# Kernel optimization log

Hardware: AMD Instinct MI355X
Metric: run time of the kernel (lower is better)

## Reference

```python
import jax, jax.numpy as jnp
import numpy as np

BN_EPS = 1e-5
INTERP_EPS = 1e-8


def _bn_relu(x, g, b, m, v):
    # eval-mode BatchNorm1d over channel dim (last axis here) + ReLU
    return jax.nn.relu((x - m) * (g / jnp.sqrt(v + BN_EPS)) + b)


def setup_inputs() -> dict:
    key = jax.random.key(0)
    ks = jax.random.split(key, 12)
    B, N, S, C1, C2 = 4, 16384, 1024, 128, 256
    Cin = C1 + C2  # 384
    H1, H2 = 256, 128
    inp = {
        "xyz1": jax.random.normal(ks[0], (B, N, 3), jnp.float32),
        "xyz2": jax.random.normal(ks[1], (B, S, 3), jnp.float32),
        "points1": jax.random.normal(ks[2], (B, N, C1), jnp.float32),
        "points2": jax.random.normal(ks[3], (B, S, C2), jnp.float32),
        # Conv1d(k=1, bias=False) weights: (out_ch, in_ch)
        "w1": jax.random.normal(ks[4], (H1, Cin), jnp.float32) * (1.0 / np.sqrt(Cin)),
        "g1": jax.random.uniform(ks[5], (H1,), jnp.float32, 0.5, 1.5),
        "b1": jax.random.normal(ks[6], (H1,), jnp.float32) * 0.1,
        "m1": jax.random.normal(ks[7], (H1,), jnp.float32) * 0.1,
        "v1": jax.random.uniform(ks[8], (H1,), jnp.float32, 0.5, 1.5),
        "w2": jax.random.normal(ks[9], (H2, H1), jnp.float32) * (1.0 / np.sqrt(H1)),
        "g2": jax.random.uniform(ks[10], (H2,), jnp.float32, 0.5, 1.5),
        "b2": jax.random.normal(ks[11], (H2,), jnp.float32) * 0.1,
        "m2": jnp.zeros((H2,), jnp.float32),
        "v2": jnp.ones((H2,), jnp.float32),
    }
    return inp


def reference(xyz1, xyz2, points1, points2, w1, g1, b1, m1, v1, w2, g2, b2, m2, v2):
    B, N, _ = xyz1.shape
    S = xyz2.shape[1]
    # squared pairwise distances (B, N, S) via ||a||^2 + ||b||^2 - 2 a.b
    sq = (
        jnp.sum(xyz1 * xyz1, -1)[:, :, None]
        + jnp.sum(xyz2 * xyz2, -1)[:, None, :]
        - 2.0 * jnp.einsum("bnd,bsd->bns", xyz1, xyz2)
    )
    neg_d, idx = jax.lax.top_k(-sq, 3)  # 3 nearest neighbors
    dists = -neg_d  # (B, N, 3) squared distances, ascending
    recip = 1.0 / (dists + INTERP_EPS)
    weight = recip / jnp.sum(recip, -1, keepdims=True)  # (B, N, 3)
    # gather neighbor features: (B, N, 3, C2)
    gathered = points2[jnp.arange(B)[:, None, None], idx]
    interpolated = jnp.einsum("bnk,bnkc->bnc", weight, gathered)
    new_points = jnp.concatenate([points1, interpolated], axis=-1)  # (B, N, Cin)
    h = _bn_relu(jnp.einsum("bnc,dc->bnd", new_points, w1), g1, b1, m1, v1)
    out = _bn_relu(jnp.einsum("bnc,dc->bnd", h, w2), g2, b2, m2, v2)
    return out
```

## Files before the change

### kernel.cpp

```cpp
#include <hip/hip_runtime.h>
#include <math.h>

#define B_    4
#define N_    16384
#define S_    1024
#define C1_   128
#define C2_   256
#define CIN_  384
#define H1_   256
#define H2_   128
#define BN_EPS_     1e-5f
#define INTERP_EPS_ 1e-8f

typedef _Float16 f16;
typedef _Float16 f16x4 __attribute__((ext_vector_type(4)));
typedef _Float16 f16x8 __attribute__((ext_vector_type(8)));
typedef float    f32x4 __attribute__((ext_vector_type(4)));
typedef unsigned int u32;

#define GLD16(g, l) \
  __builtin_amdgcn_global_load_lds((const __attribute__((address_space(1))) void*)(g), \
                                   (__attribute__((address_space(3))) void*)(l), 16, 0, 0)

#define WS_IDXP 0
#define WS_W    262144
#define WS_XI   1048576
#define WS_H    34603008
#define WS_W1F  68157440
#define WS_W2F  68354048
#define WS_SC1  68419584
#define WS_SH1  68420608
#define WS_SC2  68421632
#define WS_SH2  68422144

__global__ __launch_bounds__(256) void prep_kernel(
    const float* __restrict__ w1, const float* __restrict__ w2,
    const float* __restrict__ g1, const float* __restrict__ b1,
    const float* __restrict__ m1, const float* __restrict__ v1,
    const float* __restrict__ g2, const float* __restrict__ b2,
    const float* __restrict__ m2, const float* __restrict__ v2,
    f16* __restrict__ w1f, f16* __restrict__ w2f,
    float* __restrict__ sc1, float* __restrict__ sh1,
    float* __restrict__ sc2, float* __restrict__ sh2)
{
    const int t = blockIdx.x * 256 + threadIdx.x;
    if (t < 98304) {
        w1f[t] = (f16)w1[t];
    } else if (t < 131072) {
        w2f[t - 98304] = (f16)w2[t - 98304];
    } else if (t < 131328) {
        const int c = t - 131072;
        const float s = g1[c] / sqrtf(v1[c] + BN_EPS_);
        sc1[c] = s; sh1[c] = b1[c] - m1[c] * s;
    } else if (t < 131456) {
        const int c = t - 131328;
        const float s = g2[c] / sqrtf(v2[c] + BN_EPS_);
        sc2[c] = s; sh2[c] = b2[c] - m2[c] * s;
    }
}

__device__ __forceinline__ u32 umin_(u32 a, u32 b) { return a < b ? a : b; }
__device__ __forceinline__ u32 umax_(u32 a, u32 b) { return a > b ? a : b; }

#define KINS(k) do { \
    u32 c1 = umax_(s0, (k)); s0 = umin_(s0, (k)); \
    u32 c2 = umax_(s1, c1);  s1 = umin_(s1, c1);  \
    u32 c3 = umax_(s2, c2);  s2 = umin_(s2, c2);  \
    u32 c4 = umax_(s3, c3);  s3 = umin_(s3, c3);  \
    s4 = umin_(s4, c4); } while (0)

#define CSWAP(a_, b_) do { \
    if (rd[b_] < rd[a_] || (rd[b_] == rd[a_] && ri[b_] < ri[a_])) { \
      double td = rd[a_]; rd[a_] = rd[b_]; rd[b_] = td; \
      int ti = ri[a_]; ri[a_] = ri[b_]; ri[b_] = ti; } } while (0)

__global__ __launch_bounds__(256) void topk_kernel(
    const float* __restrict__ xyz1, const float* __restrict__ xyz2,
    u32* __restrict__ idxp_out, float* __restrict__ w_out)
{
    __shared__ float4 q[S_ + 8];
    const int b     = blockIdx.x >> 9;
    const int pbase = (blockIdx.x & 511) << 5;
    const int t     = threadIdx.x;

    for (int i = t; i < S_; i += 256) {
        const float* s = &xyz2[((size_t)b * S_ + i) * 3];
        float4 v; v.x = s[0]; v.y = s[1]; v.z = s[2]; v.w = 0.0f;
        q[i + (i >> 7)] = v;
    }
    __syncthreads();

    const int p     = pbase + (t >> 3);
    const int chunk = t & 7;
    const int qb    = chunk * 129;
    const int ebase = chunk << 7;
    const float* pp = &xyz1[((size_t)b * N_ + p) * 3];
    const float px = pp[0], py = pp[1], pz = pp[2];

    u32 s0 = 0xFFFFFFFFu, s1 = 0xFFFFFFFFu, s2 = 0xFFFFFFFFu,
        s3 = 0xFFFFFFFFu, s4 = 0xFFFFFFFFu;

    for (int i = 0; i < 128; i += 4) {
        #pragma unroll
        for (int u = 0; u < 4; ++u) {
            const float4 c = q[qb + i + u];
            const float dx = px - c.x, dy = py - c.y, dz = pz - c.z;
            const float dd = fmaf(dx, dx, fmaf(dy, dy, dz * dz));
            const u32 k = (__float_as_uint(dd) & 0xFFFFFC00u) | (u32)(ebase + i + u);
            KINS(k);
        }
    }

    #pragma unroll
    for (int msk = 1; msk <= 4; msk <<= 1) {
        u32 e0 = __shfl_xor(s0, msk), e1 = __shfl_xor(s1, msk);
        u32 e2 = __shfl_xor(s2, msk), e3 = __shfl_xor(s3, msk);
        u32 e4 = __shfl_xor(s4, msk);
        KINS(e0); KINS(e1); KINS(e2); KINS(e3); KINS(e4);
    }

    if (chunk == 0) {
        const double px6 = px, py6 = py, pz6 = pz;
        double rd[5]; int ri[5];
        const u32 ks[5] = {s0, s1, s2, s3, s4};
        #pragma unroll
        for (int j = 0; j < 5; ++j) {
            const int si = (int)(ks[j] & 1023u); ri[j] = si;
            const float4 c = q[si + (si >> 7)];
            const double dx = px6 - (double)c.x, dy = py6 - (double)c.y, dz = pz6 - (double)c.z;
            rd[j] = dx * dx + dy * dy + dz * dz;
        }
        CSWAP(0,1); CSWAP(1,2); CSWAP(0,1); CSWAP(2,3); CSWAP(1,2);
        CSWAP(0,1); CSWAP(3,4); CSWAP(2,3); CSWAP(1,2); CSWAP(0,1);
        const float r0 = 1.0f / ((float)rd[0] + INTERP_EPS_);
        const float r1 = 1.0f / ((float)rd[1] + INTERP_EPS_);
        const float r2 = 1.0f / ((float)rd[2] + INTERP_EPS_);
        const float rs = r0 + r1 + r2;
        const int row = b * N_ + p;
        idxp_out[row] = (u32)ri[0] | ((u32)ri[1] << 10) | ((u32)ri[2] << 20);
        w_out[row * 3 + 0] = r0 / rs;
        w_out[row * 3 + 1] = r1 / rs;
        w_out[row * 3 + 2] = r2 / rs;
    }
}

__global__ __launch_bounds__(256) void interp_kernel(
    const float* __restrict__ points2, const u32* __restrict__ idxp,
    const float* __restrict__ wts, f16* __restrict__ xi)
{
    const int row  = blockIdx.x * 8 + (threadIdx.x >> 5);
    const int lane = threadIdx.x & 31;
    const int bb   = row >> 14;
    const u32 u    = idxp[row];
    const int i0 = (int)(u & 1023u), i1 = (int)((u >> 10) & 1023u), i2 = (int)(u >> 20);
    const float w0 = wts[row * 3], w1w = wts[row * 3 + 1], w2w = wts[row * 3 + 2];
    const float* p2b = points2 + (size_t)bb * S_ * C2_;
    const int c0 = lane * 8;

    const float4 a0 = *(const float4*)&p2b[i0 * C2_ + c0];
    const float4 a1 = *(const float4*)&p2b[i0 * C2_ + c0 + 4];
    const float4 b0 = *(const float4*)&p2b[i1 * C2_ + c0];
    const float4 b1 = *(const float4*)&p2b[i1 * C2_ + c0 + 4];
    const float4 d0 = *(const float4*)&p2b[i2 * C2_ + c0];
    const float4 d1 = *(const float4*)&p2b[i2 * C2_ + c0 + 4];

    f16x8 o;
    o[0] = (f16)fmaf(w0, a0.x, fmaf(w1w, b0.x, w2w * d0.x));
    o[1] = (f16)fmaf(w0, a0.y, fmaf(w1w, b0.y, w2w * d0.y));
    o[2] = (f16)fmaf(w0, a0.z, fmaf(w1w, b0.z, w2w * d0.z));
    o[3] = (f16)fmaf(w0, a0.w, fmaf(w1w, b0.w, w2w * d0.w));
    o[4] = (f16)fmaf(w0, a1.x, fmaf(w1w, b1.x, w2w * d1.x));
    o[5] = (f16)fmaf(w0, a1.y, fmaf(w1w, b1.y, w2w * d1.y));
    o[6] = (f16)fmaf(w0, a1.z, fmaf(w1w, b1.z, w2w * d1.z));
    o[7] = (f16)fmaf(w0, a1.w, fmaf(w1w, b1.w, w2w * d1.w));
    *(f16x8*)&xi[(size_t)row * C2_ + c0] = o;
}

__device__ __forceinline__ void mfma_step1(const f16* As, const f16* Bs,
                                           f32x4 (&acc)[4][8],
                                           int wr, int wc, int lrow, int lhi)
{
    f16x8 af[4], bf[8];
    #pragma unroll
    for (int m = 0; m < 4; ++m)
        af[m] = *(const f16x8*)&As[(wr * 64 + m * 16 + lrow) * 32 + lhi * 8];
    #pragma unroll
    for (int n = 0; n < 8; ++n)
        bf[n] = *(const f16x8*)&Bs[(wc * 128 + n * 16 + lrow) * 32 + lhi * 8];
    #pragma unroll
    for (int m = 0; m < 4; ++m)
        #pragma unroll
        for (int n = 0; n < 8; ++n)
            acc[m][n] = __builtin_amdgcn_mfma_f32_16x16x32_f16(af[m], bf[n], acc[m][n], 0, 0, 0);
}

__global__ __launch_bounds__(256, 2) void gemm1_kernel(
    const float* __restrict__ points1, const f16* __restrict__ xi,
    const f16* __restrict__ w1f,
    const float* __restrict__ sc1v, const float* __restrict__ sh1v,
    f16* __restrict__ h)
{
    __shared__ __align__(16) f16 As[128 * 32];
    __shared__ __align__(16) f16 Bs[256 * 32];

    const int t = threadIdx.x;
    const int w = t >> 6;
    const int lane = t & 63;
    const int wr = w >> 1, wc = w & 1;
    const int lrow = lane & 15, lhi = lane >> 4;
    const int rowbase = blockIdx.x * 128;

    const int srow = t >> 1, khalf = t & 1;
    const float* p1r = points1 + (size_t)(rowbase + srow) * C1_;
    f16* asrow = &As[srow * 32 + khalf * 16];

    f32x4 acc[4][8] = {};

    for (int kb = 0; kb < C1_; kb += 32) {
        __syncthreads();
        const float* src = p1r + kb + khalf * 16;
        #pragma unroll
        for (int g4 = 0; g4 < 4; ++g4) {
            const float4 v = *(const float4*)(src + g4 * 4);
            f16x4 o = {(f16)v.x, (f16)v.y, (f16)v.z, (f16)v.w};
            *(f16x4*)(asrow + g4 * 4) = o;
        }
        #pragma unroll
        for (int j = 0; j < 4; ++j) {
            const int c = j * 256 + t;
            GLD16(w1f + (size_t)(c >> 2) * CIN_ + kb + (c & 3) * 8,
                  (char*)Bs + (j * 4096 + w * 1024));
        }
        __syncthreads();
        mfma_step1(As, Bs, acc, wr, wc, lrow, lhi);
    }

    for (int kb = C1_; kb < CIN_; kb += 32) {
        __syncthreads();
        const int kk = kb - C1_;
        #pragma unroll
        for (int j = 0; j < 2; ++j) {
            const int c = j * 256 + t;
            GLD16(xi + (size_t)(rowbase + (c >> 2)) * C2_ + kk + (c & 3) * 8,
                  (char*)As + (j * 4096 + w * 1024));
        }
        #pragma unroll
        for (int j = 0; j < 4; ++j) {
            const int c = j * 256 + t;
            GLD16(w1f + (size_t)(c >> 2) * CIN_ + kb + (c & 3) * 8,
                  (char*)Bs + (j * 4096 + w * 1024));
        }
        __syncthreads();
        mfma_step1(As, Bs, acc, wr, wc, lrow, lhi);
    }

    #pragma unroll
    for (int n = 0; n < 8; ++n) {
        const int col = wc * 128 + n * 16 + lrow;
        const float sc = sc1v[col], sh = sh1v[col];
        #pragma unroll
        for (int m = 0; m < 4; ++m) {
            const int row0 = rowbase + wr * 64 + m * 16 + lhi * 4;
            #pragma unroll
            for (int i = 0; i < 4; ++i) {
                const float v = fmaxf(fmaf(acc[m][n][i], sc, sh), 0.0f);
                h[(size_t)(row0 + i) * H1_ + col] = (f16)v;
            }
        }
    }
}

__global__ __launch_bounds__(256, 2) void gemm2_kernel(
    const f16* __restrict__ hin, const f16* __restrict__ w2f,
    const float* __restrict__ sc2v, const float* __restrict__ sh2v,
    float* __restrict__ out)
{
    __shared__ __align__(16) f16 As[128 * 32];
    __shared__ __align__(16) f16 Bs[128 * 32];

    const int t = threadIdx.x;
    const int w = t >> 6;
    const int lane = t & 63;
    const int wr = w >> 1, wc = w & 1;
    const int lrow = lane & 15, lhi = lane >> 4;
    const int rowbase = blockIdx.x * 128;

    f32x4 acc[4][4] = {};

    for (int kb = 0; kb < H1_; kb += 32) {
        __syncthreads();
        #pragma unroll
        for (int j = 0; j < 2; ++j) {
            const int c = j * 256 + t;
            GLD16(hin + (size_t)(rowbase + (c >> 2)) * H1_ + kb + (c & 3) * 8,
                  (char*)As + (j * 4096 + w * 1024));
            GLD16(w2f + (size_t)(c >> 2) * H1_ + kb + (c & 3) * 8,
                  (char*)Bs + (j * 4096 + w * 1024));
        }
        __syncthreads();
        f16x8 af[4], bf[4];
        #pragma unroll
        for (int m = 0; m < 4; ++m)
            af[m] = *(const f16x8*)&As[(wr * 64 + m * 16 + lrow) * 32 + lhi * 8];
        #pragma unroll
        for (int n = 0; n < 4; ++n)
            bf[n] = *(const f16x8*)&Bs[(wc * 64 + n * 16 + lrow) * 32 + lhi * 8];
        #pragma unroll
        for (int m = 0; m < 4; ++m)
            #pragma unroll
            for (int n = 0; n < 4; ++n)
                acc[m][n] = __builtin_amdgcn_mfma_f32_16x16x32_f16(af[m], bf[n], acc[m][n], 0, 0, 0);
    }

    #pragma unroll
    for (int n = 0; n < 4; ++n) {
        const int col = wc * 64 + n * 16 + lrow;
        const float sc = sc2v[col], sh = sh2v[col];
        #pragma unroll
        for (int m = 0; m < 4; ++m) {
            const int row0 = rowbase + wr * 64 + m * 16 + lhi * 4;
            #pragma unroll
            for (int i = 0; i < 4; ++i) {
                out[(size_t)(row0 + i) * H2_ + col] = fmaxf(fmaf(acc[m][n][i], sc, sh), 0.0f);
            }
        }
    }
}

extern "C" void kernel_launch(void* const* d_in, const int* in_sizes, int n_in,
                              void* d_out, int out_size, void* d_ws, size_t ws_size,
                              hipStream_t stream) {
    const float* xyz1    = (const float*)d_in[0];
    const float* xyz2    = (const float*)d_in[1];
    const float* points1 = (const float*)d_in[2];
    const float* points2 = (const float*)d_in[3];
    const float* w1      = (const float*)d_in[4];
    const float* g1      = (const float*)d_in[5];
    const float* b1      = (const float*)d_in[6];
    const float* m1      = (const float*)d_in[7];
    const float* v1      = (const float*)d_in[8];
    const float* w2      = (const float*)d_in[9];
    const float* g2      = (const float*)d_in[10];
    const float* b2      = (const float*)d_in[11];
    const float* m2      = (const float*)d_in[12];
    const float* v2      = (const float*)d_in[13];
    float* out = (float*)d_out;

    char* ws = (char*)d_ws;
    u32*   idxp_ws = (u32*)(ws + WS_IDXP);
    float* w_ws    = (float*)(ws + WS_W);
    f16*   xi_ws   = (f16*)(ws + WS_XI);
    f16*   h_ws    = (f16*)(ws + WS_H);
    f16*   w1f     = (f16*)(ws + WS_W1F);
    f16*   w2f     = (f16*)(ws + WS_W2F);
    float* sc1     = (float*)(ws + WS_SC1);
    float* sh1     = (float*)(ws + WS_SH1);
    float* sc2     = (float*)(ws + WS_SC2);
    float* sh2     = (float*)(ws + WS_SH2);

    topk_kernel<<<dim3(B_ * (N_ / 32)), dim3(256), 0, stream>>>(xyz1, xyz2, idxp_ws, w_ws);
    prep_kernel<<<dim3(514), dim3(256), 0, stream>>>(w1, w2, g1, b1, m1, v1,
                                                     g2, b2, m2, v2,
                                                     w1f, w2f, sc1, sh1, sc2, sh2);
    interp_kernel<<<dim3(B_ * N_ / 8), dim3(256), 0, stream>>>(points2, idxp_ws, w_ws, xi_ws);
    gemm1_kernel<<<dim3(512), dim3(256), 0, stream>>>(points1, xi_ws, w1f, sc1, sh1, h_ws);
    gemm2_kernel<<<dim3(512), dim3(256), 0, stream>>>(h_ws, w2f, sc2, sh2, out);
}
```

Measured before the change: 185.9 us.

## Double-buffer LDS tiles in both GEMM kernels to overlap loads with MFMA

Both GEMM kernels now use two LDS buffers per operand. The next K-slice is issued (global_load_lds for weights, xi and h, and register prefetch for points1) before the MFMAs run on the current slice, so only one barrier per step remains. This is meant to hide global-memory latency behind compute. In exchange it doubles LDS use (gemm1 grows to 48KB per block), which could limit occupancy, and it relies on the barrier covering the async LDS loads.

```diff
diff --git a/kernel.cpp b/kernel.cpp
--- a/kernel.cpp
+++ b/kernel.cpp
@@ -200,8 +200,8 @@
     const float* __restrict__ sc1v, const float* __restrict__ sh1v,
     f16* __restrict__ h)
 {
-    __shared__ __align__(16) f16 As[128 * 32];
-    __shared__ __align__(16) f16 Bs[256 * 32];
+    __shared__ __align__(16) f16 As[2 * 128 * 32];
+    __shared__ __align__(16) f16 Bs[2 * 256 * 32];
 
     const int t = threadIdx.x;
     const int w = t >> 6;
@@ -212,46 +212,74 @@
 
     const int srow = t >> 1, khalf = t & 1;
     const float* p1r = points1 + (size_t)(rowbase + srow) * C1_;
-    f16* asrow = &As[srow * 32 + khalf * 16];
 
     f32x4 acc[4][8] = {};
-
-    for (int kb = 0; kb < C1_; kb += 32) {
-        __syncthreads();
-        const float* src = p1r + kb + khalf * 16;
-        #pragma unroll
-        for (int g4 = 0; g4 < 4; ++g4) {
-            const float4 v = *(const float4*)(src + g4 * 4);
-            f16x4 o = {(f16)v.x, (f16)v.y, (f16)v.z, (f16)v.w};
-            *(f16x4*)(asrow + g4 * 4) = o;
-        }
+    float4 pre0, pre1, pre2, pre3;
+
+    {
+        const float* src = p1r + khalf * 16;
+        pre0 = *(const float4*)(src + 0);
+        pre1 = *(const float4*)(src + 4);
+        pre2 = *(const float4*)(src + 8);
+        pre3 = *(const float4*)(src + 12);
+        f16* asrow = As + srow * 32 + khalf * 16;
+        f16x4 o0 = {(f16)pre0.x, (f16)pre0.y, (f16)pre0.z, (f16)pre0.w};
+        f16x4 o1 = {(f16)pre1.x, (f16)pre1.y, (f16)pre1.z, (f16)pre1.w};
+        f16x4 o2 = {(f16)pre2.x, (f16)pre2.y, (f16)pre2.z, (f16)pre2.w};
+        f16x4 o3 = {(f16)pre3.x, (f16)pre3.y, (f16)pre3.z, (f16)pre3.w};
+        *(f16x4*)(asrow + 0) = o0; *(f16x4*)(asrow + 4) = o1;
+        *(f16x4*)(asrow + 8) = o2; *(f16x4*)(asrow + 12) = o3;
         #pragma unroll
         for (int j = 0; j < 4; ++j) {
             const int c = j * 256 + t;
-            GLD16(w1f + (size_t)(c >> 2) * CIN_ + kb + (c & 3) * 8,
+            GLD16(w1f + (size_t)(c >> 2) * CIN_ + (c & 3) * 8,
                   (char*)Bs + (j * 4096 + w * 1024));
         }
+    }
+    __syncthreads();
+
+    for (int step = 0; step < 12; ++step) {
+        const int pb = step & 1, nb = pb ^ 1;
+        const int nkb = (step + 1) * 32;
+        const bool has_next = (step < 11);
+        const bool nextA = (nkb < C1_);
+
+        if (has_next) {
+            if (nextA) {
+                const float* src = p1r + nkb + khalf * 16;
+                pre0 = *(const float4*)(src + 0);
+                pre1 = *(const float4*)(src + 4);
+                pre2 = *(const float4*)(src + 8);
+                pre3 = *(const float4*)(src + 12);
+            } else {
+                const int kk = nkb - C1_;
+                #pragma unroll
+                for (int j = 0; j < 2; ++j) {
+                    const int c = j * 256 + t;
+                    GLD16(xi + (size_t)(rowbase + (c >> 2)) * C2_ + kk + (c & 3) * 8,
+                          (char*)As + (nb * 8192 + j * 4096 + w * 1024));
+                }
+            }
+            #pragma unroll
+            for (int j = 0; j < 4; ++j) {
+                const int c = j * 256 + t;
+                GLD16(w1f + (size_t)(c >> 2) * CIN_ + nkb + (c & 3) * 8,
+                      (char*)Bs + (nb * 16384 + j * 4096 + w * 1024));
+            }
+        }
+
+        mfma_step1(As + pb * 4096, Bs + pb * 8192, acc, wr, wc, lrow, lhi);
+
+        if (has_next && nextA) {
+            f16* asrow = As + nb * 4096 + srow * 32 + khalf * 16;
+            f16x4 o0 = {(f16)pre0.x, (f16)pre0.y, (f16)pre0.z, (f16)pre0.w};
+            f16x4 o1 = {(f16)pre1.x, (f16)pre1.y, (f16)pre1.z, (f16)pre1.w};
+            f16x4 o2 = {(f16)pre2.x, (f16)pre2.y, (f16)pre2.z, (f16)pre2.w};
+            f16x4 o3 = {(f16)pre3.x, (f16)pre3.y, (f16)pre3.z, (f16)pre3.w};
+            *(f16x4*)(asrow + 0) = o0; *(f16x4*)(asrow + 4) = o1;
+            *(f16x4*)(asrow + 8) = o2; *(f16x4*)(asrow + 12) = o3;
+        }
         __syncthreads();
-        mfma_step1(As, Bs, acc, wr, wc, lrow, lhi);
-    }
-
-    for (int kb = C1_; kb < CIN_; kb += 32) {
-        __syncthreads();
-        const int kk = kb - C1_;
-        #pragma unroll
-        for (int j = 0; j < 2; ++j) {
-            const int c = j * 256 + t;
-            GLD16(xi + (size_t)(rowbase + (c >> 2)) * C2_ + kk + (c & 3) * 8,
-                  (char*)As + (j * 4096 + w * 1024));
-        }
-        #pragma unroll
-        for (int j = 0; j < 4; ++j) {
-            const int c = j * 256 + t;
-            GLD16(w1f + (size_t)(c >> 2) * CIN_ + kb + (c & 3) * 8,
-                  (char*)Bs + (j * 4096 + w * 1024));
-        }
-        __syncthreads();
-        mfma_step1(As, Bs, acc, wr, wc, lrow, lhi);
     }
 
     #pragma unroll
@@ -275,8 +303,8 @@
     const float* __restrict__ sc2v, const float* __restrict__ sh2v,
     float* __restrict__ out)
 {
-    __shared__ __align__(16) f16 As[128 * 32];
-    __shared__ __align__(16) f16 Bs[128 * 32];
+    __shared__ __align__(16) f16 As[2 * 128 * 32];
+    __shared__ __align__(16) f16 Bs[2 * 128 * 32];
 
     const int t = threadIdx.x;
     const int w = t >> 6;
@@ -287,29 +315,47 @@
 
     f32x4 acc[4][4] = {};
 
-    for (int kb = 0; kb < H1_; kb += 32) {
-        __syncthreads();
-        #pragma unroll
-        for (int j = 0; j < 2; ++j) {
-            const int c = j * 256 + t;
-            GLD16(hin + (size_t)(rowbase + (c >> 2)) * H1_ + kb + (c & 3) * 8,
-                  (char*)As + (j * 4096 + w * 1024));
-            GLD16(w2f + (size_t)(c >> 2) * H1_ + kb + (c & 3) * 8,
-                  (char*)Bs + (j * 4096 + w * 1024));
-        }
-        __syncthreads();
+    #pragma unroll
+    for (int j = 0; j < 2; ++j) {
+        const int c = j * 256 + t;
+        GLD16(hin + (size_t)(rowbase + (c >> 2)) * H1_ + (c & 3) * 8,
+              (char*)As + (j * 4096 + w * 1024));
+        GLD16(w2f + (size_t)(c >> 2) * H1_ + (c & 3) * 8,
+              (char*)Bs + (j * 4096 + w * 1024));
+    }
+    __syncthreads();
+
+    for (int step = 0; step < 8; ++step) {
+        const int pb = step & 1, nb = pb ^ 1;
+        const int nkb = (step + 1) * 32;
+
+        if (step < 7) {
+            #pragma unroll
+            for (int j = 0; j < 2; ++j) {
+                const int c = j * 256 + t;
+                GLD16(hin + (size_t)(rowbase + (c >> 2)) * H1_ + nkb + (c & 3) * 8,
+                      (char*)As + (nb * 8192 + j * 4096 + w * 1024));
+                GLD16(w2f + (size_t)(c >> 2) * H1_ + nkb + (c & 3) * 8,
+                      (char*)Bs + (nb * 8192 + j * 4096 + w * 1024));
+            }
+        }
+
+        const f16* Ac = As + pb * 4096;
+        const f16* Bc = Bs + pb * 4096;
         f16x8 af[4], bf[4];
         #pragma unroll
         for (int m = 0; m < 4; ++m)
-            af[m] = *(const f16x8*)&As[(wr * 64 + m * 16 + lrow) * 32 + lhi * 8];
+            af[m] = *(const f16x8*)&Ac[(wr * 64 + m * 16 + lrow) * 32 + lhi * 8];
         #pragma unroll
         for (int n = 0; n < 4; ++n)
-            bf[n] = *(const f16x8*)&Bs[(wc * 64 + n * 16 + lrow) * 32 + lhi * 8];
+            bf[n] = *(const f16x8*)&Bc[(wc * 64 + n * 16 + lrow) * 32 + lhi * 8];
         #pragma unroll
         for (int m = 0; m < 4; ++m)
             #pragma unroll
             for (int n = 0; n < 4; ++n)
                 acc[m][n] = __builtin_amdgcn_mfma_f32_16x16x32_f16(af[m], bf[n], acc[m][n], 0, 0, 0);
+
+        __syncthreads();
     }
 
     #pragma unroll
```

New measurement: 187.6 us. No clear change (+0.9%).
